# Performance work log

Measured on AMD Instinct MI355X. Metric: run time of the kernel, lower is better.

Reference implementation:

```python
import jax, jax.numpy as jnp
import numpy as np

B, L, D, N = 16, 512, 768, 8192


def setup_inputs() -> dict:
    key = jax.random.key(0)
    k = jax.random.split(key, 5)
    return {
        "y": jax.random.normal(k[0], (B, L, D), dtype=jnp.float32),
        "Wy_w": jax.random.normal(k[1], (D, D), dtype=jnp.float32) * 0.02,
        "Wy_b": jnp.zeros((D,), dtype=jnp.float32),
        "Wz_w": jax.random.normal(k[2], (D, D), dtype=jnp.float32) * 0.02,
        "Wz_b": jnp.zeros((D,), dtype=jnp.float32),
        "dic_z": jax.random.normal(k[3], (N, D), dtype=jnp.float32),
        "prior": jax.random.uniform(k[4], (N,), dtype=jnp.float32),
    }


def reference(y, Wy_w, Wy_b, Wz_w, Wz_b, dic_z, prior):
    # y: [B,L,D]; dic_z: [N,D]; prior: [N]
    d = y.shape[-1]
    qy = jnp.einsum('bld,ed->ble', y, Wy_w) + Wy_b          # Wy(y): [B,L,D]
    kz = jnp.einsum('nd,ed->ne', dic_z, Wz_w) + Wz_b        # Wz(dic_z): [N,D]
    scores = jnp.einsum('bld,nd->bln', qy, kz) / jnp.sqrt(jnp.float32(d))
    attn = jax.nn.softmax(scores, axis=-1)                   # [B,L,N]
    # z[b,l,d] = sum_n prior[n] * attn[b,l,n] * dic_z[n,d]
    # == (attn * prior) @ dic_z, avoiding the [L,N,D] intermediate.
    z = jnp.einsum('bln,nd->bld', attn * prior, dic_z)       # [B,L,D]
    return z
```

## Files before the change

kernel.cpp:

```cpp
#include <hip/hip_runtime.h>
#include <stdint.h>

#define M_ 8192
#define D_ 768
#define N_ 8192

typedef unsigned short u16;
typedef __attribute__((ext_vector_type(8))) unsigned short us8;
typedef __attribute__((ext_vector_type(8))) __bf16 bf16x8;
typedef __attribute__((ext_vector_type(4))) float f32x4;

__device__ __forceinline__ u16 f2bf(float f) {
  uint32_t u = __builtin_bit_cast(uint32_t, f);
  u += 0x7FFFu + ((u >> 16) & 1u);
  return (u16)(u >> 16);
}
__device__ __forceinline__ float bf2f(u16 u) {
  return __builtin_bit_cast(float, ((uint32_t)u) << 16);
}

__device__ __forceinline__ void gload_lds16(const void* g, void* l) {
  __builtin_amdgcn_global_load_lds(
      (__attribute__((address_space(1))) void*)g,
      (__attribute__((address_space(3))) void*)l, 16, 0, 0);
}

__global__ __launch_bounds__(256)
void k_cvt_bf16(const float* __restrict__ in, u16* __restrict__ out, int n4) {
  int stride = gridDim.x * blockDim.x;
  for (int i = blockIdx.x * blockDim.x + threadIdx.x; i < n4; i += stride) {
    float4 v = reinterpret_cast<const float4*>(in)[i];
    ushort4 o;
    o.x = f2bf(v.x); o.y = f2bf(v.y); o.z = f2bf(v.z); o.w = f2bf(v.w);
    reinterpret_cast<ushort4*>(out)[i] = o;
  }
}

__global__ __launch_bounds__(256)
void k_build_vt(const float* __restrict__ dic, const float* __restrict__ prior,
                u16* __restrict__ Vt) {
  __shared__ float t[32][33];
  const int n0 = blockIdx.x * 32, d0 = blockIdx.y * 32;
  const int tx = threadIdx.x, ty = threadIdx.y;
  #pragma unroll
  for (int i = ty; i < 32; i += 8)
    t[i][tx] = dic[(size_t)(n0 + i) * D_ + d0 + tx] * prior[n0 + i];
  __syncthreads();
  #pragma unroll
  for (int i = ty; i < 32; i += 8)
    Vt[(size_t)(d0 + i) * N_ + n0 + tx] = f2bf(t[tx][i]);
}

template<int EP>
__global__ __launch_bounds__(512, 2)
void k_gemm8(const u16* __restrict__ A, const u16* __restrict__ Bm,
             u16* __restrict__ Cb, float* __restrict__ Cf, float scale,
             long ldk, int K, int Ncols, int nbx, int tps, long partStride) {
  extern __shared__ u16 ldsu[];
  const int tid = threadIdx.x;
  const int lane = tid & 63, wid = tid >> 6;
  const int wr = wid >> 2, wc = wid & 3;
  const int L15 = lane & 15, L7 = lane & 7, g = lane >> 4;

  const int nwg = gridDim.x;
  const int bid = blockIdx.x;
  const int wg = ((nwg & 7) == 0) ? ((bid & 7) * (nwg >> 3) + (bid >> 3)) : bid;
  const int s = wg / tps;
  const int r = wg % tps;
  const int bx = r % nbx, by = r / nbx;
  const long m0 = (long)by * 256;
  const long n0 = (long)bx * 256;
  const int NT = K >> 6;

  int aBase[2], bBase[2];
  #pragma unroll
  for (int ks = 0; ks < 2; ++ks) {
    const int slot = (((ks * 4 + g) ^ L7) << 3);
    aBase[ks] = wr * 8192 + L15 * 64 + slot;
    bBase[ks] = 16384 + (wc >> 1) * 8192 + (wc & 1) * 4096 + L15 * 64 + slot;
  }

  const int rowoff = wid * 8 + (lane >> 3);
  const int colsw = ((lane & 7) ^ (lane >> 3)) << 3;
  const u16* Ag = A + m0 * ldk + (long)s * K;
  const u16* Bg = Bm + n0 * ldk + (long)s * K;
  u16* ldsW = ldsu + tid * 8;

  auto stage = [&](int q) {
    if (q >= 4 * NT) return;
    const int j = q >> 2;
    const int buf = j & 1, mat = (q >> 1) & 1, half = q & 1;
    const u16* src = (mat ? Bg : Ag) + (size_t)(half * 128 + rowoff) * ldk + j * 64 + colsw;
    u16* dst = ldsW + buf * 32768 + mat * 16384 + half * 8192;
    gload_lds16(src, dst);
    gload_lds16(src + (size_t)64 * ldk, dst + 4096);
  };

  for (int q = 0; q < 7; ++q) stage(q);
  asm volatile("s_waitcnt vmcnt(6)" ::: "memory");
  __builtin_amdgcn_s_barrier();

  f32x4 acc[8][4] = {};

  for (int k = 0; k < NT; ++k) {
    const int bufOff = (k & 1) * 32768;
    bf16x8 afr[8][2], bfr[4][2];
    __builtin_amdgcn_sched_barrier(0);
    #pragma unroll
    for (int ks = 0; ks < 2; ++ks) {
      #pragma unroll
      for (int j = 0; j < 4; ++j)
        bfr[j][ks] = __builtin_bit_cast(bf16x8,
            *reinterpret_cast<const us8*>(&ldsu[bufOff + bBase[ks] + j * 1024]));
      #pragma unroll
      for (int i = 0; i < 8; ++i)
        afr[i][ks] = __builtin_bit_cast(bf16x8,
            *reinterpret_cast<const us8*>(&ldsu[bufOff + aBase[ks] + i * 1024]));
    }
    __builtin_amdgcn_sched_barrier(0);

    #pragma unroll
    for (int ph = 0; ph < 4; ++ph) {
      stage(4 * k + 7 + ph);
      __builtin_amdgcn_s_barrier();
      if (ph == 0) {
        asm volatile("s_waitcnt lgkmcnt(0)" ::: "memory");
        __builtin_amdgcn_sched_barrier(0);
      }
      if (ph == 3) {
        if (k < NT - 2) asm volatile("s_waitcnt vmcnt(6)" ::: "memory");
        else            asm volatile("s_waitcnt vmcnt(0)" ::: "memory");
      }
      __builtin_amdgcn_s_setprio(1);
      #pragma unroll
      for (int i = 2 * ph; i < 2 * ph + 2; ++i)
        #pragma unroll
        for (int j = 0; j < 4; ++j)
          #pragma unroll
          for (int ks = 0; ks < 2; ++ks)
            acc[i][j] = __builtin_amdgcn_mfma_f32_16x16x32_bf16(
                afr[i][ks], bfr[j][ks], acc[i][j], 0, 0, 0);
      __builtin_amdgcn_s_setprio(0);
      __builtin_amdgcn_s_barrier();
      __builtin_amdgcn_sched_barrier(0);
    }
  }

  #pragma unroll
  for (int i = 0; i < 8; ++i)
    #pragma unroll
    for (int j = 0; j < 4; ++j)
      #pragma unroll
      for (int q = 0; q < 4; ++q) {
        long row = m0 + wr * 128 + i * 16 + ((lane >> 4) * 4) + q;
        long col = n0 + wc * 64 + j * 16 + L15;
        if (EP == 0) Cb[row * (long)Ncols + col] = f2bf(acc[i][j][q] * scale);
        else         Cf[(long)s * partStride + row * (long)Ncols + col] = acc[i][j][q];
      }
}

__global__ __launch_bounds__(256)
void k_reduce2(const float* __restrict__ part, long partStride,
               const float* __restrict__ linv, float* __restrict__ out, int n4) {
  int stride = gridDim.x * blockDim.x;
  const float4* p0 = reinterpret_cast<const float4*>(part);
  const float4* p1 = reinterpret_cast<const float4*>(part + partStride);
  for (int i = blockIdx.x * blockDim.x + threadIdx.x; i < n4; i += stride) {
    float4 a = p0[i], b = p1[i];
    float sc = linv[(i * 4) / D_];
    float4 o;
    o.x = (a.x + b.x) * sc; o.y = (a.y + b.y) * sc;
    o.z = (a.z + b.z) * sc; o.w = (a.w + b.w) * sc;
    reinterpret_cast<float4*>(out)[i] = o;
  }
}

template<int EP>
__global__ __launch_bounds__(256, 2)
void k_gemm_nt(const u16* __restrict__ A, const u16* __restrict__ Bm,
               float* __restrict__ Cf, u16* __restrict__ Cb,
               const float* __restrict__ bias, const float* __restrict__ rowscale,
               float scale, int N, int K) {
  __shared__ u16 Al[128 * 64];
  __shared__ u16 Bl[128 * 64];
  const int tid = threadIdx.x;
  const int lane = tid & 63;
  const int wave = tid >> 6;
  const int wr = wave >> 1, wc = wave & 1;
  const long m0 = (long)blockIdx.y * 128;
  const long n0 = (long)blockIdx.x * 128;

  f32x4 acc[4][4] = {};

  const u16* gA = A + (m0 + (tid >> 3)) * (long)K + (tid & 7) * 8;
  const u16* gB = Bm + (n0 + (tid >> 3)) * (long)K + (tid & 7) * 8;

  for (int kt = 0; kt < K; kt += 64) {
    __syncthreads();
    #pragma unroll
    for (int r = 0; r < 4; ++r) {
      gload_lds16(gA + (size_t)(r * 32) * K + kt, &Al[r * 2048 + tid * 8]);
      gload_lds16(gB + (size_t)(r * 32) * K + kt, &Bl[r * 2048 + tid * 8]);
    }
    __syncthreads();
    #pragma unroll
    for (int ks = 0; ks < 2; ++ks) {
      bf16x8 av[4], bv[4];
      #pragma unroll
      for (int i = 0; i < 4; ++i) {
        av[i] = __builtin_bit_cast(bf16x8, *reinterpret_cast<const us8*>(
            &Al[(wr * 64 + i * 16 + (lane & 15)) * 64 + ks * 32 + (lane >> 4) * 8]));
        bv[i] = __builtin_bit_cast(bf16x8, *reinterpret_cast<const us8*>(
            &Bl[(wc * 64 + i * 16 + (lane & 15)) * 64 + ks * 32 + (lane >> 4) * 8]));
      }
      #pragma unroll
      for (int i = 0; i < 4; ++i)
        #pragma unroll
        for (int j = 0; j < 4; ++j)
          acc[i][j] = __builtin_amdgcn_mfma_f32_16x16x32_bf16(av[i], bv[j], acc[i][j], 0, 0, 0);
    }
  }

  #pragma unroll
  for (int i = 0; i < 4; ++i) {
    #pragma unroll
    for (int j = 0; j < 4; ++j) {
      #pragma unroll
      for (int q = 0; q < 4; ++q) {
        long row = m0 + wr * 64 + i * 16 + ((lane >> 4) * 4) + q;
        long col = n0 + wc * 64 + j * 16 + (lane & 15);
        float v = acc[i][j][q];
        if (EP == 1)      Cb[row * N + col] = f2bf(v + bias[col]);
        else if (EP == 2) Cb[row * N + col] = f2bf(v * scale);
        else              Cf[row * N + col] = v * rowscale[row];
      }
    }
  }
}

__global__ __launch_bounds__(256)
void k_softmax(u16* __restrict__ S, float* __restrict__ linv) {
  const int row = blockIdx.x;
  u16* rp = S + (size_t)row * N_;
  const int tid = threadIdx.x;
  float v[32];
  #pragma unroll
  for (int c = 0; c < 4; ++c) {
    us8 u = *reinterpret_cast<const us8*>(rp + (size_t)(c * 256 + tid) * 8);
    #pragma unroll
    for (int q = 0; q < 8; ++q) v[c * 8 + q] = bf2f(u[q]);
  }
  float mx = v[0];
  #pragma unroll
  for (int i = 1; i < 32; ++i) mx = fmaxf(mx, v[i]);
  #pragma unroll
  for (int o = 1; o < 64; o <<= 1) mx = fmaxf(mx, __shfl_xor(mx, o));
  __shared__ float red[8];
  if ((tid & 63) == 0) red[tid >> 6] = mx;
  __syncthreads();
  mx = fmaxf(fmaxf(red[0], red[1]), fmaxf(red[2], red[3]));
  float s = 0.f;
  #pragma unroll
  for (int i = 0; i < 32; ++i) { v[i] = __expf(v[i] - mx); s += v[i]; }
  #pragma unroll
  for (int o = 1; o < 64; o <<= 1) s += __shfl_xor(s, o);
  if ((tid & 63) == 0) red[4 + (tid >> 6)] = s;
  __syncthreads();
  s = (red[4] + red[5]) + (red[6] + red[7]);
  #pragma unroll
  for (int c = 0; c < 4; ++c) {
    us8 u;
    #pragma unroll
    for (int q = 0; q < 8; ++q) u[q] = f2bf(v[c * 8 + q]);
    *reinterpret_cast<us8*>(rp + (size_t)(c * 256 + tid) * 8) = u;
  }
  if (tid == 0) linv[row] = 1.0f / s;
}

extern "C" void kernel_launch(void* const* d_in, const int* in_sizes, int n_in,
                              void* d_out, int out_size, void* d_ws, size_t ws_size,
                              hipStream_t stream) {
  (void)in_sizes; (void)n_in; (void)out_size;
  const float* y     = (const float*)d_in[0];
  const float* Wy_w  = (const float*)d_in[1];
  const float* Wy_b  = (const float*)d_in[2];
  const float* Wz_w  = (const float*)d_in[3];
  const float* Wz_b  = (const float*)d_in[4];
  const float* dic   = (const float*)d_in[5];
  const float* prior = (const float*)d_in[6];
  float* out = (float*)d_out;

  hipFuncSetAttribute(reinterpret_cast<const void*>(&k_gemm8<0>),
                      hipFuncAttributeMaxDynamicSharedMemorySize, 131072);
  hipFuncSetAttribute(reinterpret_cast<const void*>(&k_gemm8<1>),
                      hipFuncAttributeMaxDynamicSharedMemorySize, 131072);

  char* base = (char*)d_ws;
  size_t off = 0;
  auto alloc = [&](size_t bytes) -> char* {
    char* p = base + off;
    off = (off + bytes + 255) & ~(size_t)255;
    return p;
  };
  u16*  Yb   = (u16*)alloc((size_t)M_ * D_ * 2);
  u16*  Db   = (u16*)alloc((size_t)N_ * D_ * 2);
  u16*  Wyb  = (u16*)alloc((size_t)D_ * D_ * 2);
  u16*  Wzb  = (u16*)alloc((size_t)D_ * D_ * 2);
  u16*  Qb   = (u16*)alloc((size_t)M_ * D_ * 2);
  u16*  Kb   = (u16*)alloc((size_t)N_ * D_ * 2);
  u16*  Vt   = (u16*)alloc((size_t)D_ * N_ * 2);
  float* linv = (float*)alloc((size_t)M_ * 4);
  size_t fixed = off;
  int Mc = M_;
  while (Mc > 256 &&
         fixed + (size_t)Mc * N_ * 2 + 2 * (size_t)Mc * D_ * 4 > ws_size)
    Mc >>= 1;
  u16*   Sc   = (u16*)alloc((size_t)Mc * N_ * 2);
  float* part = (float*)alloc(2 * (size_t)Mc * D_ * 4);
  const long partStride = (long)Mc * D_;

  auto cvt = [&](const float* src, u16* dst, size_t n) {
    int n4 = (int)(n / 4);
    int blocks = (n4 + 255) / 256;
    if (blocks > 2048) blocks = 2048;
    hipLaunchKernelGGL(k_cvt_bf16, dim3(blocks), dim3(256), 0, stream, src, dst, n4);
  };
  cvt(y,    Yb,  (size_t)M_ * D_);
  cvt(dic,  Db,  (size_t)N_ * D_);
  cvt(Wy_w, Wyb, (size_t)D_ * D_);
  cvt(Wz_w, Wzb, (size_t)D_ * D_);

  hipLaunchKernelGGL(k_build_vt, dim3(N_ / 32, D_ / 32), dim3(32, 8), 0, stream,
                     dic, prior, Vt);

  hipLaunchKernelGGL(HIP_KERNEL_NAME(k_gemm_nt<1>), dim3(D_ / 128, M_ / 128), dim3(256), 0, stream,
                     Yb, Wyb, (float*)nullptr, Qb, Wy_b, (const float*)nullptr, 0.f, D_, D_);
  hipLaunchKernelGGL(HIP_KERNEL_NAME(k_gemm_nt<1>), dim3(D_ / 128, N_ / 128), dim3(256), 0, stream,
                     Db, Wzb, (float*)nullptr, Kb, Wz_b, (const float*)nullptr, 0.f, D_, D_);

  const float scale = 0.036084391824351615f;
  for (int mc = 0; mc < M_; mc += Mc) {
    {
      const int nbx = N_ / 256, nby = Mc / 256;
      hipLaunchKernelGGL(HIP_KERNEL_NAME(k_gemm8<0>), dim3(nbx * nby), dim3(512), 131072, stream,
                         Qb + (size_t)mc * D_, Kb, Sc, (float*)nullptr, scale,
                         (long)D_, D_, N_, nbx, nbx * nby, 0L);
    }
    hipLaunchKernelGGL(k_softmax, dim3(Mc), dim3(256), 0, stream, Sc, linv + mc);
    {
      const int nbx = D_ / 256, nby = Mc / 256, tps = nbx * nby;
      hipLaunchKernelGGL(HIP_KERNEL_NAME(k_gemm8<1>), dim3(tps * 2), dim3(512), 131072, stream,
                         Sc, Vt, (u16*)nullptr, part, 1.0f,
                         (long)N_, N_ / 2, D_, nbx, tps, partStride);
    }
    {
      int n4 = Mc * D_ / 4;
      int blocks = (n4 + 255) / 256;
      if (blocks > 2048) blocks = 2048;
      hipLaunchKernelGGL(k_reduce2, dim3(blocks), dim3(256), 0, stream,
                         part, partStride, linv + mc, out + (size_t)mc * D_, n4);
    }
  }
}
```

Measured before the change: 359.2 us.

## Interleave per-phase A fragment LDS reads and reorder global prefetch schedule

The bf16 GEMM main loop no longer loads all A and B fragments from LDS at the start of each K tile. B fragments are now read once per tile and A fragments per phase, two row blocks at a time, which cuts register pressure for the fragments. The global-to-LDS prefetch is split into single loads issued per phase in a new order, so the next tile's A half and the tile-after-next's B are staged earlier. This aims to overlap LDS reads with MFMA work and ease register use, but adds an LDS wait and a barrier inside every phase and relies on delicate wait-count correctness.

```diff
diff --git a/kernel.cpp b/kernel.cpp
--- a/kernel.cpp
+++ b/kernel.cpp
@@ -86,60 +86,72 @@
   const u16* Bg = Bm + n0 * ldk + (long)s * K;
   u16* ldsW = ldsu + tid * 8;
 
-  auto stage = [&](int q) {
-    if (q >= 4 * NT) return;
-    const int j = q >> 2;
-    const int buf = j & 1, mat = (q >> 1) & 1, half = q & 1;
-    const u16* src = (mat ? Bg : Ag) + (size_t)(half * 128 + rowoff) * ldk + j * 64 + colsw;
-    u16* dst = ldsW + buf * 32768 + mat * 16384 + half * 8192;
-    gload_lds16(src, dst);
-    gload_lds16(src + (size_t)64 * ldk, dst + 4096);
+  auto g1 = [&](int t, int mat, int r0) {
+    if (t >= NT) return;
+    const u16* src = (mat ? Bg : Ag) + (size_t)(r0 + rowoff) * ldk
+                     + (size_t)t * 64 + colsw;
+    gload_lds16(src, ldsW + (t & 1) * 32768 + mat * 16384 + (r0 >> 6) * 512 * 8);
   };
 
-  for (int q = 0; q < 7; ++q) stage(q);
+  g1(0, 1, 0); g1(0, 1, 64); g1(0, 1, 128); g1(0, 1, 192);
+  g1(0, 0, 0); g1(0, 0, 128);
+  g1(0, 0, 64); g1(0, 0, 192);
+  g1(1, 1, 0); g1(1, 1, 64); g1(1, 1, 128); g1(1, 1, 192);
+  g1(1, 0, 0); g1(1, 0, 128);
   asm volatile("s_waitcnt vmcnt(6)" ::: "memory");
   __builtin_amdgcn_s_barrier();
 
   f32x4 acc[8][4] = {};
+  bf16x8 bfr[4][2];
 
   for (int k = 0; k < NT; ++k) {
     const int bufOff = (k & 1) * 32768;
-    bf16x8 afr[8][2], bfr[4][2];
-    __builtin_amdgcn_sched_barrier(0);
-    #pragma unroll
-    for (int ks = 0; ks < 2; ++ks) {
-      #pragma unroll
-      for (int j = 0; j < 4; ++j)
-        bfr[j][ks] = __builtin_bit_cast(bf16x8,
-            *reinterpret_cast<const us8*>(&ldsu[bufOff + bBase[ks] + j * 1024]));
-      #pragma unroll
-      for (int i = 0; i < 8; ++i)
-        afr[i][ks] = __builtin_bit_cast(bf16x8,
-            *reinterpret_cast<const us8*>(&ldsu[bufOff + aBase[ks] + i * 1024]));
-    }
-    __builtin_amdgcn_sched_barrier(0);
 
     #pragma unroll
     for (int ph = 0; ph < 4; ++ph) {
-      stage(4 * k + 7 + ph);
-      __builtin_amdgcn_s_barrier();
+      bf16x8 afr[2][2];
       if (ph == 0) {
-        asm volatile("s_waitcnt lgkmcnt(0)" ::: "memory");
-        __builtin_amdgcn_sched_barrier(0);
-      }
-      if (ph == 3) {
-        if (k < NT - 2) asm volatile("s_waitcnt vmcnt(6)" ::: "memory");
-        else            asm volatile("s_waitcnt vmcnt(0)" ::: "memory");
-      }
-      __builtin_amdgcn_s_setprio(1);
-      #pragma unroll
-      for (int i = 2 * ph; i < 2 * ph + 2; ++i)
         #pragma unroll
         for (int j = 0; j < 4; ++j)
           #pragma unroll
           for (int ks = 0; ks < 2; ++ks)
-            acc[i][j] = __builtin_amdgcn_mfma_f32_16x16x32_bf16(
-                afr[i][ks], bfr[j][ks], acc[i][j], 0, 0, 0);
+            bfr[j][ks] = __builtin_bit_cast(bf16x8,
+                *reinterpret_cast<const us8*>(&ldsu[bufOff + bBase[ks] + j * 1024]));
+      }
+      #pragma unroll
+      for (int t = 0; t < 2; ++t)
+        #pragma unroll
+        for (int ks = 0; ks < 2; ++ks)
+          afr[t][ks] = __builtin_bit_cast(bf16x8,
+              *reinterpret_cast<const us8*>(
+                  &ldsu[bufOff + aBase[ks] + (2 * ph + t) * 1024]));
+      __builtin_amdgcn_sched_barrier(0);
+
+      if (ph == 0)      { g1(k + 1, 0, 64);  g1(k + 1, 0, 192); }
+      else if (ph == 1) { g1(k + 2, 1, 0);   g1(k + 2, 1, 64);  }
+      else if (ph == 2) { g1(k + 2, 1, 128); g1(k + 2, 1, 192); }
+      else              { g1(k + 2, 0, 0);   g1(k + 2, 0, 128); }
+
+      if (ph == 0)
+        asm volatile("s_waitcnt lgkmcnt(8)" ::: "memory");
+      __builtin_amdgcn_s_barrier();
+      asm volatile("s_waitcnt lgkmcnt(0)" ::: "memory");
+      __builtin_amdgcn_sched_barrier(0);
+      if (ph == 3) {
+        if (k < NT - 2) asm volatile("s_waitcnt vmcnt(6)" ::: "memory");
+        else            asm volatile("s_waitcnt vmcnt(0)" ::: "memory");
+        __builtin_amdgcn_sched_barrier(0);
+      }
+
+      __builtin_amdgcn_s_setprio(1);
+      #pragma unroll
+      for (int t = 0; t < 2; ++t)
+        #pragma unroll
+        for (int j = 0; j < 4; ++j)
+          #pragma unroll
+          for (int ks = 0; ks < 2; ++ks)
+            acc[2 * ph + t][j] = __builtin_amdgcn_mfma_f32_16x16x32_bf16(
+                afr[t][ks], bfr[j][ks], acc[2 * ph + t][j], 0, 0, 0);
       __builtin_amdgcn_s_setprio(0);
       __builtin_amdgcn_s_barrier();
       __builtin_amdgcn_sched_barrier(0);
```

After: 351.3 us. 1.02x faster.

## Shrink GEMM K-tile to 32 and simplify double-buffered pipeline

Applied to the files above, without the earlier changes.

The 256x256 bf16 GEMM kernel now steps through K in chunks of 32 instead of 64. This halves LDS use to 64 KB with a new XOR swizzle, and the four-phase interleaved schedule is replaced by a simple double buffer: load fragments, barrier, issue the next prefetch, barrier, then run all MFMAs. The smaller LDS footprint could allow more resident workgroups, and the simpler schedule cuts scheduling complexity. In exchange there are twice as many iterations, each with two barriers and less MFMA work, so load latency may be exposed more and there is less overlap within an iteration.

```diff
diff --git a/kernel.cpp b/kernel.cpp
--- a/kernel.cpp
+++ b/kernel.cpp
@@ -53,14 +53,14 @@
 
 template<int EP>
 __global__ __launch_bounds__(512, 2)
-void k_gemm8(const u16* __restrict__ A, const u16* __restrict__ Bm,
-             u16* __restrict__ Cb, float* __restrict__ Cf, float scale,
-             long ldk, int K, int Ncols, int nbx, int tps, long partStride) {
+void k_gemm32(const u16* __restrict__ A, const u16* __restrict__ Bm,
+              u16* __restrict__ Cb, float* __restrict__ Cf, float scale,
+              long ldk, int K, int Ncols, int nbx, int tps, long partStride) {
   extern __shared__ u16 ldsu[];
   const int tid = threadIdx.x;
   const int lane = tid & 63, wid = tid >> 6;
   const int wr = wid >> 2, wc = wid & 3;
-  const int L15 = lane & 15, L7 = lane & 7, g = lane >> 4;
+  const int L15 = lane & 15, g = lane >> 4;
 
   const int nwg = gridDim.x;
   const int bid = blockIdx.x;
@@ -70,80 +70,65 @@
   const int bx = r % nbx, by = r / nbx;
   const long m0 = (long)by * 256;
   const long n0 = (long)bx * 256;
-  const int NT = K >> 6;
-
-  int aBase[2], bBase[2];
-  #pragma unroll
-  for (int ks = 0; ks < 2; ++ks) {
-    const int slot = (((ks * 4 + g) ^ L7) << 3);
-    aBase[ks] = wr * 8192 + L15 * 64 + slot;
-    bBase[ks] = 16384 + (wc >> 1) * 8192 + (wc & 1) * 4096 + L15 * 64 + slot;
-  }
-
-  const int rowoff = wid * 8 + (lane >> 3);
-  const int colsw = ((lane & 7) ^ (lane >> 3)) << 3;
+  const int NT = K >> 5;
+
+  const int swz = (L15 >> 1) & 3;
+  const int aslot = (g ^ swz) * 8;
+  const int aBase = (wr * 128 + L15) * 32 + aslot;
+  const int bBase = 8192 + (wc * 64 + L15) * 32 + aslot;
+
+  const int rowoff = tid >> 2;
+  const int slotsrc = (((tid & 3) ^ ((tid >> 3) & 3))) * 8;
   const u16* Ag = A + m0 * ldk + (long)s * K;
   const u16* Bg = Bm + n0 * ldk + (long)s * K;
   u16* ldsW = ldsu + tid * 8;
 
-  auto stage = [&](int q) {
-    if (q >= 4 * NT) return;
-    const int j = q >> 2;
-    const int buf = j & 1, mat = (q >> 1) & 1, half = q & 1;
-    const u16* src = (mat ? Bg : Ag) + (size_t)(half * 128 + rowoff) * ldk + j * 64 + colsw;
-    u16* dst = ldsW + buf * 32768 + mat * 16384 + half * 8192;
-    gload_lds16(src, dst);
-    gload_lds16(src + (size_t)64 * ldk, dst + 4096);
+  auto stage = [&](int t) {
+    if (t >= NT) return;
+    const long co = (long)t * 32 + slotsrc;
+    const int db = (t & 1) * 16384;
+    gload_lds16(Ag + (size_t)rowoff * ldk + co,          ldsW + db);
+    gload_lds16(Ag + (size_t)(128 + rowoff) * ldk + co,  ldsW + db + 4096);
+    gload_lds16(Bg + (size_t)rowoff * ldk + co,          ldsW + db + 8192);
+    gload_lds16(Bg + (size_t)(128 + rowoff) * ldk + co,  ldsW + db + 12288);
   };
 
-  for (int q = 0; q < 7; ++q) stage(q);
-  asm volatile("s_waitcnt vmcnt(6)" ::: "memory");
+  stage(0); stage(1);
+  asm volatile("s_waitcnt vmcnt(4)" ::: "memory");
   __builtin_amdgcn_s_barrier();
 
   f32x4 acc[8][4] = {};
 
   for (int k = 0; k < NT; ++k) {
-    const int bufOff = (k & 1) * 32768;
-    bf16x8 afr[8][2], bfr[4][2];
+    const int bufOff = (k & 1) * 16384;
+    bf16x8 afr[8], bfr[4];
+    #pragma unroll
+    for (int j = 0; j < 4; ++j)
+      bfr[j] = __builtin_bit_cast(bf16x8,
+          *reinterpret_cast<const us8*>(&ldsu[bufOff + bBase + j * 512]));
+    #pragma unroll
+    for (int i = 0; i < 8; ++i)
+      afr[i] = __builtin_bit_cast(bf16x8,
+          *reinterpret_cast<const us8*>(&ldsu[bufOff + aBase + i * 512]));
+    asm volatile("s_waitcnt lgkmcnt(0)" ::: "memory");
     __builtin_amdgcn_sched_barrier(0);
-    #pragma unroll
-    for (int ks = 0; ks < 2; ++ks) {
+    __builtin_amdgcn_s_barrier();
+
+    stage(k + 2);
+    if (k < NT - 2) asm volatile("s_waitcnt vmcnt(4)" ::: "memory");
+    else            asm volatile("s_waitcnt vmcnt(0)" ::: "memory");
+    __builtin_amdgcn_sched_barrier(0);
+    __builtin_amdgcn_s_barrier();
+    __builtin_amdgcn_sched_barrier(0);
+
+    __builtin_amdgcn_s_setprio(1);
+    #pragma unroll
+    for (int i = 0; i < 8; ++i)
       #pragma unroll
       for (int j = 0; j < 4; ++j)
-        bfr[j][ks] = __builtin_bit_cast(bf16x8,
-            *reinterpret_cast<const us8*>(&ldsu[bufOff + bBase[ks] + j * 1024]));
-      #pragma unroll
-      for (int i = 0; i < 8; ++i)
-        afr[i][ks] = __builtin_bit_cast(bf16x8,
-            *reinterpret_cast<const us8*>(&ldsu[bufOff + aBase[ks] + i * 1024]));
-    }
-    __builtin_amdgcn_sched_barrier(0);
-
-    #pragma unroll
-    for (int ph = 0; ph < 4; ++ph) {
-      stage(4 * k + 7 + ph);
-      __builtin_amdgcn_s_barrier();
-      if (ph == 0) {
-        asm volatile("s_waitcnt lgkmcnt(0)" ::: "memory");
-        __builtin_amdgcn_sched_barrier(0);
-      }
-      if (ph == 3) {
-        if (k < NT - 2) asm volatile("s_waitcnt vmcnt(6)" ::: "memory");
-        else            asm volatile("s_waitcnt vmcnt(0)" ::: "memory");
-      }
-      __builtin_amdgcn_s_setprio(1);
-      #pragma unroll
-      for (int i = 2 * ph; i < 2 * ph + 2; ++i)
-        #pragma unroll
-        for (int j = 0; j < 4; ++j)
-          #pragma unroll
-          for (int ks = 0; ks < 2; ++ks)
-            acc[i][j] = __builtin_amdgcn_mfma_f32_16x16x32_bf16(
-                afr[i][ks], bfr[j][ks], acc[i][j], 0, 0, 0);
-      __builtin_amdgcn_s_setprio(0);
-      __builtin_amdgcn_s_barrier();
-      __builtin_amdgcn_sched_barrier(0);
-    }
+        acc[i][j] = __builtin_amdgcn_mfma_f32_16x16x32_bf16(
+            afr[i], bfr[j], acc[i][j], 0, 0, 0);
+    __builtin_amdgcn_s_setprio(0);
   }
 
   #pragma unroll
@@ -290,10 +275,10 @@
   const float* prior = (const float*)d_in[6];
   float* out = (float*)d_out;
 
-  hipFuncSetAttribute(reinterpret_cast<const void*>(&k_gemm8<0>),
-                      hipFuncAttributeMaxDynamicSharedMemorySize, 131072);
-  hipFuncSetAttribute(reinterpret_cast<const void*>(&k_gemm8<1>),
-                      hipFuncAttributeMaxDynamicSharedMemorySize, 131072);
+  hipFuncSetAttribute(reinterpret_cast<const void*>(&k_gemm32<0>),
+                      hipFuncAttributeMaxDynamicSharedMemorySize, 65536);
+  hipFuncSetAttribute(reinterpret_cast<const void*>(&k_gemm32<1>),
+                      hipFuncAttributeMaxDynamicSharedMemorySize, 65536);
 
   char* base = (char*)d_ws;
   size_t off = 0;
@@ -342,14 +327,14 @@
   for (int mc = 0; mc < M_; mc += Mc) {
     {
       const int nbx = N_ / 256, nby = Mc / 256;
-      hipLaunchKernelGGL(HIP_KERNEL_NAME(k_gemm8<0>), dim3(nbx * nby), dim3(512), 131072, stream,
+      hipLaunchKernelGGL(HIP_KERNEL_NAME(k_gemm32<0>), dim3(nbx * nby), dim3(512), 65536, stream,
                          Qb + (size_t)mc * D_, Kb, Sc, (float*)nullptr, scale,
                          (long)D_, D_, N_, nbx, nbx * nby, 0L);
     }
     hipLaunchKernelGGL(k_softmax, dim3(Mc), dim3(256), 0, stream, Sc, linv + mc);
     {
       const int nbx = D_ / 256, nby = Mc / 256, tps = nbx * nby;
-      hipLaunchKernelGGL(HIP_KERNEL_NAME(k_gemm8<1>), dim3(tps * 2), dim3(512), 131072, stream,
+      hipLaunchKernelGGL(HIP_KERNEL_NAME(k_gemm32<1>), dim3(tps * 2), dim3(512), 65536, stream,
                          Sc, Vt, (u16*)nullptr, part, 1.0f,
                          (long)N_, N_ / 2, D_, nbx, tps, partStride);
     }
```

New measurement: 363.8 us. About the same (+1.3%).

## Software-pipeline LDS fragment reads with MFMA in the bf16 GEMM main loop

Applied to the files above, without the earlier changes.

Rewrites the main loop of the 256x256 bf16 GEMM so A fragments are read from LDS in small chunks interleaved with MFMA phases, and the next tile's B and first A fragments are prefetched into ping-pong registers before the last MFMA phase. Global-to-LDS staging now issues a whole K-tile per step, eight loads per thread, instead of quarter-tile staging spread over phases. The goal is to hide LDS read latency behind matrix math and cut barriers per tile. The B LDS layout is simplified to match the new load order. The cost is more live fragment registers and an unrolled-by-two loop that assumes NT is even.

```diff
diff --git a/kernel.cpp b/kernel.cpp
--- a/kernel.cpp
+++ b/kernel.cpp
@@ -53,7 +53,7 @@
 
 template<int EP>
 __global__ __launch_bounds__(512, 2)
-void k_gemm8(const u16* __restrict__ A, const u16* __restrict__ Bm,
+void k_gemmP(const u16* __restrict__ A, const u16* __restrict__ Bm,
              u16* __restrict__ Cb, float* __restrict__ Cf, float scale,
              long ldk, int K, int Ncols, int nbx, int tps, long partStride) {
   extern __shared__ u16 ldsu[];
@@ -77,7 +77,7 @@
   for (int ks = 0; ks < 2; ++ks) {
     const int slot = (((ks * 4 + g) ^ L7) << 3);
     aBase[ks] = wr * 8192 + L15 * 64 + slot;
-    bBase[ks] = 16384 + (wc >> 1) * 8192 + (wc & 1) * 4096 + L15 * 64 + slot;
+    bBase[ks] = 16384 + wc * 4096 + L15 * 64 + slot;
   }
 
   const int rowoff = wid * 8 + (lane >> 3);
@@ -86,65 +86,76 @@
   const u16* Bg = Bm + n0 * ldk + (long)s * K;
   u16* ldsW = ldsu + tid * 8;
 
-  auto stage = [&](int q) {
-    if (q >= 4 * NT) return;
-    const int j = q >> 2;
-    const int buf = j & 1, mat = (q >> 1) & 1, half = q & 1;
-    const u16* src = (mat ? Bg : Ag) + (size_t)(half * 128 + rowoff) * ldk + j * 64 + colsw;
-    u16* dst = ldsW + buf * 32768 + mat * 16384 + half * 8192;
-    gload_lds16(src, dst);
-    gload_lds16(src + (size_t)64 * ldk, dst + 4096);
+  auto stage = [&](int t) {
+    if (t >= NT) return;
+    const long co = (long)t * 64 + colsw;
+    u16* db = ldsW + (t & 1) * 32768;
+    #pragma unroll
+    for (int c = 0; c < 4; ++c)
+      gload_lds16(Ag + (size_t)(c * 64 + rowoff) * ldk + co, db + c * 4096);
+    #pragma unroll
+    for (int c = 0; c < 4; ++c)
+      gload_lds16(Bg + (size_t)(c * 64 + rowoff) * ldk + co, db + 16384 + c * 4096);
   };
 
-  for (int q = 0; q < 7; ++q) stage(q);
-  asm volatile("s_waitcnt vmcnt(6)" ::: "memory");
+#define SB __builtin_amdgcn_sched_barrier(0)
+#define LGKM(n) asm volatile("s_waitcnt lgkmcnt(" #n ")" ::: "memory")
+#define RDA(dst, bo, q)                                                      \
+  _Pragma("unroll") for (int t_ = 0; t_ < 2; ++t_)                           \
+    _Pragma("unroll") for (int ks_ = 0; ks_ < 2; ++ks_)                      \
+      dst[t_][ks_] = __builtin_bit_cast(bf16x8,                              \
+          *reinterpret_cast<const us8*>(                                     \
+              &ldsu[(bo) + aBase[ks_] + (2 * (q) + t_) * 1024]));
+#define RDB(dst, bo)                                                         \
+  _Pragma("unroll") for (int j_ = 0; j_ < 4; ++j_)                           \
+    _Pragma("unroll") for (int ks_ = 0; ks_ < 2; ++ks_)                      \
+      dst[j_][ks_] = __builtin_bit_cast(bf16x8,                              \
+          *reinterpret_cast<const us8*>(                                     \
+              &ldsu[(bo) + bBase[ks_] + j_ * 1024]));
+#define MMA(p, asrc, bsrc)                                                   \
+  __builtin_amdgcn_s_setprio(1);                                             \
+  _Pragma("unroll") for (int t_ = 0; t_ < 2; ++t_)                           \
+    _Pragma("unroll") for (int j_ = 0; j_ < 4; ++j_)                         \
+      _Pragma("unroll") for (int ks_ = 0; ks_ < 2; ++ks_)                    \
+        acc[2 * (p) + t_][j_] = __builtin_amdgcn_mfma_f32_16x16x32_bf16(     \
+            asrc[t_][ks_], bsrc[j_][ks_], acc[2 * (p) + t_][j_], 0, 0, 0);   \
+  __builtin_amdgcn_s_setprio(0);
+
+#define TILE(TP, bC, bN, t)                                                  \
+  {                                                                          \
+    const int bo_ = (TP) * 32768, boN_ = ((TP) ^ 1) * 32768;                 \
+    RDA(aY, bo_, 1); SB; LGKM(4); SB; MMA(0, aX, bC);                        \
+    RDA(aX, bo_, 2); SB; LGKM(4); SB; MMA(1, aY, bC);                        \
+    RDA(aY, bo_, 3); SB; LGKM(4); SB; MMA(2, aX, bC);                        \
+    LGKM(0); SB;                                                             \
+    __builtin_amdgcn_s_barrier(); SB;                                        \
+    stage((t) + 2); SB;                                                      \
+    if ((t) + 2 < NT) { asm volatile("s_waitcnt vmcnt(8)" ::: "memory"); }   \
+    else              { asm volatile("s_waitcnt vmcnt(0)" ::: "memory"); }   \
+    SB;                                                                      \
+    __builtin_amdgcn_s_barrier(); SB;                                        \
+    if ((t) + 1 < NT) { RDB(bN, boN_); RDA(aX, boN_, 0); }                   \
+    SB; MMA(3, aY, bC);                                                      \
+  }
+
+  stage(0); stage(1);
+  asm volatile("s_waitcnt vmcnt(8)" ::: "memory");
   __builtin_amdgcn_s_barrier();
 
   f32x4 acc[8][4] = {};
-
-  for (int k = 0; k < NT; ++k) {
-    const int bufOff = (k & 1) * 32768;
-    bf16x8 afr[8][2], bfr[4][2];
-    __builtin_amdgcn_sched_barrier(0);
-    #pragma unroll
-    for (int ks = 0; ks < 2; ++ks) {
-      #pragma unroll
-      for (int j = 0; j < 4; ++j)
-        bfr[j][ks] = __builtin_bit_cast(bf16x8,
-            *reinterpret_cast<const us8*>(&ldsu[bufOff + bBase[ks] + j * 1024]));
-      #pragma unroll
-      for (int i = 0; i < 8; ++i)
-        afr[i][ks] = __builtin_bit_cast(bf16x8,
-            *reinterpret_cast<const us8*>(&ldsu[bufOff + aBase[ks] + i * 1024]));
-    }
-    __builtin_amdgcn_sched_barrier(0);
-
-    #pragma unroll
-    for (int ph = 0; ph < 4; ++ph) {
-      stage(4 * k + 7 + ph);
-      __builtin_amdgcn_s_barrier();
-      if (ph == 0) {
-        asm volatile("s_waitcnt lgkmcnt(0)" ::: "memory");
-        __builtin_amdgcn_sched_barrier(0);
-      }
-      if (ph == 3) {
-        if (k < NT - 2) asm volatile("s_waitcnt vmcnt(6)" ::: "memory");
-        else            asm volatile("s_waitcnt vmcnt(0)" ::: "memory");
-      }
-      __builtin_amdgcn_s_setprio(1);
-      #pragma unroll
-      for (int i = 2 * ph; i < 2 * ph + 2; ++i)
-        #pragma unroll
-        for (int j = 0; j < 4; ++j)
-          #pragma unroll
-          for (int ks = 0; ks < 2; ++ks)
-            acc[i][j] = __builtin_amdgcn_mfma_f32_16x16x32_bf16(
-                afr[i][ks], bfr[j][ks], acc[i][j], 0, 0, 0);
-      __builtin_amdgcn_s_setprio(0);
-      __builtin_amdgcn_s_barrier();
-      __builtin_amdgcn_sched_barrier(0);
-    }
-  }
+  bf16x8 aX[2][2], aY[2][2], bA_[4][2], bB_[4][2];
+  RDB(bA_, 0); RDA(aX, 0, 0);
+
+  for (int k = 0; k < NT; k += 2) {
+    TILE(0, bA_, bB_, k);
+    TILE(1, bB_, bA_, k + 1);
+  }
+#undef SB
+#undef LGKM
+#undef RDA
+#undef RDB
+#undef MMA
+#undef TILE
 
   #pragma unroll
   for (int i = 0; i < 8; ++i)
@@ -290,9 +301,9 @@
   const float* prior = (const float*)d_in[6];
   float* out = (float*)d_out;
 
-  hipFuncSetAttribute(reinterpret_cast<const void*>(&k_gemm8<0>),
+  hipFuncSetAttribute(reinterpret_cast<const void*>(&k_gemmP<0>),
                       hipFuncAttributeMaxDynamicSharedMemorySize, 131072);
-  hipFuncSetAttribute(reinterpret_cast<const void*>(&k_gemm8<1>),
+  hipFuncSetAttribute(reinterpret_cast<const void*>(&k_gemmP<1>),
                       hipFuncAttributeMaxDynamicSharedMemorySize, 131072);
 
   char* base = (char*)d_ws;
@@ -342,14 +353,14 @@
   for (int mc = 0; mc < M_; mc += Mc) {
     {
       const int nbx = N_ / 256, nby = Mc / 256;
-      hipLaunchKernelGGL(HIP_KERNEL_NAME(k_gemm8<0>), dim3(nbx * nby), dim3(512), 131072, stream,
+      hipLaunchKernelGGL(HIP_KERNEL_NAME(k_gemmP<0>), dim3(nbx * nby), dim3(512), 131072, stream,
                          Qb + (size_t)mc * D_, Kb, Sc, (float*)nullptr, scale,
                          (long)D_, D_, N_, nbx, nbx * nby, 0L);
     }
     hipLaunchKernelGGL(k_softmax, dim3(Mc), dim3(256), 0, stream, Sc, linv + mc);
     {
       const int nbx = D_ / 256, nby = Mc / 256, tps = nbx * nby;
-      hipLaunchKernelGGL(HIP_KERNEL_NAME(k_gemm8<1>), dim3(tps * 2), dim3(512), 131072, stream,
+      hipLaunchKernelGGL(HIP_KERNEL_NAME(k_gemmP<1>), dim3(tps * 2), dim3(512), 131072, stream,
                          Sc, Vt, (u16*)nullptr, part, 1.0f,
                          (long)N_, N_ / 2, D_, nbx, tps, partStride);
     }
```

Result: slower. 457.9 us (+27.5%).
